# Kernel tuning notes

Measured on AMD Instinct MI355X. Metric: run time of the kernel, lower is better.

The kernel has to match this reference:

```python
import jax, jax.numpy as jnp
import numpy as np

B, L, D = 4, 2048, 512


def setup_inputs() -> dict:
    key = jax.random.key(0)
    ks = jax.random.split(key, 12)
    f32 = jnp.float32
    mk = lambda k, s: jax.random.normal(k, s, dtype=f32)
    # xavier-uniform-ish init scale for the linear weights
    w_qkv_lim = np.sqrt(6.0 / (6 * D + 6 * D)).astype(np.float32)
    w_out_lim = np.sqrt(6.0 / (2 * D + 2 * D)).astype(np.float32)
    return {
        "q_real": mk(ks[0], (B, L, D)),
        "q_imag": mk(ks[1], (B, L, D)),
        "k_real": mk(ks[2], (B, L, D)),
        "k_imag": mk(ks[3], (B, L, D)),
        "v_real": mk(ks[4], (B, L, D)),
        "v_imag": mk(ks[5], (B, L, D)),
        "pad_mask": jax.random.randint(ks[6], (B, L), 0, 2).astype(jnp.bool_),
        "W_qkv": jax.random.uniform(ks[7], (6 * D, 6 * D), f32, -w_qkv_lim, w_qkv_lim),
        "b_qkv": jnp.zeros((6 * D,), f32),
        "W_out": jax.random.uniform(ks[8], (2 * D, 2 * D), f32, -w_out_lim, w_out_lim),
        "b_out": jnp.zeros((2 * D,), f32),
    }


def reference(q_real, q_imag, k_real, k_imag, v_real, v_imag, pad_mask,
              W_qkv, b_qkv, W_out, b_out):
    b, l, d = q_real.shape
    # fused QKV projection over concatenated real/imag streams: [B, L, 6D]
    x = jnp.concatenate([q_real, q_imag, k_real, k_imag, v_real, v_imag], axis=-1)
    qkv = x @ W_qkv.T + b_qkv                      # torch Linear: x @ W^T + b
    qkv = qkv.reshape(b, l, 6, d)
    q_r, k_r = qkv[:, :, 0], qkv[:, :, 2]
    v_r, v_i = qkv[:, :, 4], qkv[:, :, 5]
    scale = jnp.asarray(d, jnp.float32) ** -0.5
    scores = jnp.einsum('bqd,bkd->bqk', q_r, k_r) * scale   # [B, L, L]
    scores = jnp.where(pad_mask[:, None, :], -jnp.inf, scores)
    attn = jax.nn.softmax(scores, axis=-1)         # dropout omitted (eval mode)
    out_real = jnp.einsum('bqk,bkd->bqd', attn, v_r)
    out_imag = jnp.einsum('bqk,bkd->bqd', attn, v_i)
    out = jnp.concatenate([out_real, out_imag], axis=-1) @ W_out.T + b_out
    return out[..., :d], out[..., d:]
```

## Files before the change

kernel.cpp:

```cpp
#include <hip/hip_runtime.h>
#include <cstdint>
#include <cstddef>

typedef unsigned short ushort;
typedef __attribute__((ext_vector_type(8))) short short8;
typedef __attribute__((ext_vector_type(16))) float f32x16;

__device__ __forceinline__ float bf2f(ushort u) {
  union { unsigned u; float f; } c; c.u = ((unsigned)u) << 16; return c.f;
}
__device__ __forceinline__ ushort f2bf(float f) {
  union { float f; unsigned u; } c; c.f = f;
  unsigned u = c.u;
  return (ushort)((u + 0x7fffu + ((u >> 16) & 1u)) >> 16);
}

#define G2L(g, l) __builtin_amdgcn_global_load_lds( \
    (const __attribute__((address_space(1))) void*)(g), \
    (__attribute__((address_space(3))) void*)(l), 16, 0, 0)

#define BARRIER() do { asm volatile("" ::: "memory"); __builtin_amdgcn_s_barrier(); asm volatile("" ::: "memory"); } while (0)
#define LGKM0()   do { asm volatile("s_waitcnt lgkmcnt(0)" ::: "memory"); __builtin_amdgcn_sched_barrier(0); } while (0)

struct MArgs {
  const ushort* A; int lda; long asz;
  const ushort* B; int ldb; long bsz;
  void* C; int ldc; long csz;
  int K;
  const float* bias;
  float* C2;
};

template<int MODE, int BN>
__launch_bounds__(512, 1)
__global__ void mfma_gemm(MArgs g) {
  constexpr int BM = 256;
  constexpr int WN = BN / 64;
  constexpr int WM = 8 / WN;
  constexpr int WMSZ = BM / WM;
  constexpr int MF = WMSZ / 32;
  constexpr int NBG = BN / 64;
  constexpr int LPS = 4 + NBG;

  __shared__ __attribute__((aligned(16))) ushort As[2][BM * 64];
  __shared__ __attribute__((aligned(16))) ushort Bs[2][BN * 64];

  const int tid = threadIdx.x;
  const int lane = tid & 63;
  const int wave = tid >> 6;
  const int z = blockIdx.z;

  int bx = blockIdx.x, by = blockIdx.y;
  {
    const int gx = gridDim.x;
    const int nwg = gx * gridDim.y;
    int wg = by * gx + bx;
    wg = (wg & 7) * (nwg >> 3) + (wg >> 3);
    bx = wg % gx; by = wg / gx;
  }
  const long m0 = (long)by * BM;
  const long n0 = (long)bx * BN;
  const ushort* Ab = g.A + (long)z * g.asz;
  const ushort* Bb = g.B + (long)z * g.bsz;

  const int srow = tid >> 3;
  const long skel = (long)((((tid & 7) - srow) & 7) * 8);
  const ushort* ga[4];
  const ushort* gb[NBG];
#pragma unroll
  for (int q = 0; q < 4; ++q) ga[q] = Ab + (m0 + q * 64 + srow) * (long)g.lda + skel;
#pragma unroll
  for (int q = 0; q < NBG; ++q) gb[q] = Bb + (n0 + q * 64 + srow) * (long)g.ldb + skel;

  const int l31 = lane & 31, hb = lane >> 5;
  const int wmi = wave / WN, wni = wave % WN;
  int aoff[MF], arot[MF];
#pragma unroll
  for (int mf = 0; mf < MF; ++mf) {
    const int r = wmi * WMSZ + mf * 32 + l31;
    aoff[mf] = r * 64;
    arot[mf] = (r + hb) & 7;
  }
  int boff[2], brot[2];
#pragma unroll
  for (int nf = 0; nf < 2; ++nf) {
    const int r = wni * 64 + nf * 32 + l31;
    boff[nf] = r * 64;
    brot[nf] = (r + hb) & 7;
  }

  f32x16 acc[MF][2];
#pragma unroll
  for (int mf = 0; mf < MF; ++mf)
#pragma unroll
    for (int nf = 0; nf < 2; ++nf)
#pragma unroll
      for (int r = 0; r < 16; ++r) acc[mf][nf][r] = 0.f;

  auto STAGE_A = [&](int buf, int t) {
    const long ko = (long)t * 64;
#pragma unroll
    for (int q = 0; q < 4; ++q) G2L(ga[q] + ko, &As[buf][q * 4096 + tid * 8]);
  };
  auto STAGE_B = [&](int buf, int t) {
    const long ko = (long)t * 64;
#pragma unroll
    for (int q = 0; q < NBG; ++q) G2L(gb[q] + ko, &Bs[buf][q * 4096 + tid * 8]);
  };

  STAGE_A(0, 0); STAGE_B(0, 0);
  STAGE_A(1, 1); STAGE_B(1, 1);
  asm volatile("s_waitcnt vmcnt(%0)" :: "n"(LPS) : "memory");
  BARRIER();

  const int nt = g.K >> 6;
  int cur = 0;
  for (int t = 0; t < nt; ++t) {
    const ushort* as = &As[cur][0];
    const ushort* bs = &Bs[cur][0];
    short8 av[4][MF], bv[4][2];

#define READ_H(h) do { \
  _Pragma("unroll") for (int mf = 0; mf < MF; ++mf) \
    av[h][mf] = *(const short8*)(as + aoff[mf] + (((2 * (h) + arot[mf]) & 7) << 3)); \
  _Pragma("unroll") for (int nf = 0; nf < 2; ++nf) \
    bv[h][nf] = *(const short8*)(bs + boff[nf] + (((2 * (h) + brot[nf]) & 7) << 3)); \
} while (0)
#define MFMA_H(h) do { \
  __builtin_amdgcn_s_setprio(1); \
  _Pragma("unroll") for (int mf = 0; mf < MF; ++mf) \
  _Pragma("unroll") for (int nf = 0; nf < 2; ++nf) \
    acc[mf][nf] = __builtin_amdgcn_mfma_f32_32x32x16_bf16(av[h][mf], bv[h][nf], acc[mf][nf], 0, 0, 0); \
  __builtin_amdgcn_s_setprio(0); \
} while (0)

    READ_H(0); READ_H(1);
    MFMA_H(0);
    BARRIER();

    READ_H(2); READ_H(3);
    MFMA_H(1);
    LGKM0();
    BARRIER();

    if (t + 2 < nt) STAGE_A(cur, t + 2);
    MFMA_H(2);
    BARRIER();

    if (t + 2 < nt) STAGE_B(cur, t + 2);
    MFMA_H(3);
    if (t + 1 < nt) {
      if (t + 2 < nt) asm volatile("s_waitcnt vmcnt(%0)" :: "n"(LPS) : "memory");
      else            asm volatile("s_waitcnt vmcnt(0)" ::: "memory");
      BARRIER();
    }
    cur ^= 1;
#undef READ_H
#undef MFMA_H
  }

  const int cc = l31;
  const int rbase = 4 * hb;
  ushort* Cu = (ushort*)g.C + (long)z * g.csz;
  float* Cf = (float*)g.C;
#pragma unroll
  for (int mf = 0; mf < MF; ++mf) {
#pragma unroll
    for (int nf = 0; nf < 2; ++nf) {
      const long col = n0 + wni * 64 + nf * 32 + cc;
      float bsv = 0.f;
      if (MODE == 0 || MODE == 3) bsv = g.bias[col];
#pragma unroll
      for (int r = 0; r < 16; ++r) {
        const long row = m0 + wmi * WMSZ + mf * 32 + (r & 3) + 8 * (r >> 2) + rbase;
        float v = acc[mf][nf][r] + bsv;
        if (MODE == 3) {
          float* dst = (col < 512) ? (Cf + row * 512 + col) : (g.C2 + row * 512 + (col - 512));
          *dst = v;
        } else {
          Cu[row * (long)g.ldc + col] = f2bf(v);
        }
      }
    }
  }
}

__global__ void cvt_x6(const float* x0, const float* x1, const float* x2,
                       const float* x3, const float* x4, const float* x5, ushort* X) {
  const long m = blockIdx.y;
  const int c4 = (blockIdx.x * 256 + threadIdx.x) * 4;
  const int p = c4 >> 9, d = c4 & 511;
  const float* xp;
  switch (p) {
    case 0: xp = x0; break; case 1: xp = x1; break; case 2: xp = x2; break;
    case 3: xp = x3; break; case 4: xp = x4; break; default: xp = x5; break;
  }
  float4 v = *(const float4*)(xp + m * 512 + d);
  ushort4 o; o.x = f2bf(v.x); o.y = f2bf(v.y); o.z = f2bf(v.z); o.w = f2bf(v.w);
  *(ushort4*)(X + m * 3072 + c4) = o;
}

__device__ __forceinline__ int chunk_map(int c) { return (c == 0) ? 0 : (c == 1) ? 2 : (c == 2) ? 4 : 5; }

__global__ void cvt_w4(const float* W, ushort* Wq4) {
  const long r = blockIdx.y;
  const int c4 = (blockIdx.x * 256 + threadIdx.x) * 4;
  const long wr = (long)chunk_map((int)(r >> 9)) * 512 + (r & 511);
  float4 v = *(const float4*)(W + wr * 3072 + c4);
  ushort4 o; o.x = f2bf(v.x); o.y = f2bf(v.y); o.z = f2bf(v.z); o.w = f2bf(v.w);
  *(ushort4*)(Wq4 + r * 3072 + c4) = o;
}

__global__ void cvt_wout(const float* W, ushort* Wo) {
  const long r = blockIdx.y;
  const int c4 = threadIdx.x * 4;
  float4 v = *(const float4*)(W + r * 1024 + c4);
  ushort4 o; o.x = f2bf(v.x); o.y = f2bf(v.y); o.z = f2bf(v.z); o.w = f2bf(v.w);
  *(ushort4*)(Wo + r * 1024 + c4) = o;
}

__global__ void mk_bias4(const float* bqkv, float* b4) {
  const int n = blockIdx.x * 256 + threadIdx.x;
  b4[n] = bqkv[chunk_map(n >> 9) * 512 + (n & 511)];
}

__global__ void transpose_v(const ushort* QKV, ushort* Vt) {
  __shared__ ushort t[64][65];
  const int tid = threadIdx.x;
  const int k0 = blockIdx.x * 64, n0 = blockIdx.y * 64, b = blockIdx.z;
  const ushort* src = QKV + (long)b * 2048 * 2048 + 1024;
#pragma unroll
  for (int i = 0; i < 16; ++i) {
    int idx = i * 256 + tid; int r = idx >> 6, c = idx & 63;
    t[r][c] = src[(long)(k0 + r) * 2048 + (n0 + c)];
  }
  __syncthreads();
  ushort* dst = Vt + (long)b * 1024 * 2048;
#pragma unroll
  for (int i = 0; i < 16; ++i) {
    int idx = i * 256 + tid; int r = idx >> 6, c = idx & 63;
    dst[(long)(n0 + r) * 2048 + (k0 + c)] = t[c][r];
  }
}

__launch_bounds__(256)
__global__ void softmax_rows(ushort* S, const int* mask) {
  const int lane = threadIdx.x & 63;
  const int wave = threadIdx.x >> 6;
  const long row = (long)blockIdx.x * 4 + wave;
  const int* m = mask + (row >> 11) * 2048 + lane * 32;
  ushort* s = S + row * 2048 + lane * 32;
  const float scale = 0.04419417382415922f;

  short8 raw[4];
#pragma unroll
  for (int i = 0; i < 4; ++i) raw[i] = *(const short8*)(s + i * 8);
  int4 mi[8];
#pragma unroll
  for (int i = 0; i < 8; ++i) mi[i] = *(const int4*)(m + i * 4);

  float v[32];
  int mk[32];
#pragma unroll
  for (int i = 0; i < 8; ++i) {
    mk[i * 4 + 0] = mi[i].x; mk[i * 4 + 1] = mi[i].y;
    mk[i * 4 + 2] = mi[i].z; mk[i * 4 + 3] = mi[i].w;
  }
#pragma unroll
  for (int i = 0; i < 32; ++i) v[i] = bf2f((ushort)raw[i >> 3][i & 7]) * scale;

  float mx = -INFINITY;
#pragma unroll
  for (int i = 0; i < 32; ++i) if (!mk[i]) mx = fmaxf(mx, v[i]);
#pragma unroll
  for (int off = 32; off; off >>= 1) mx = fmaxf(mx, __shfl_xor(mx, off));

  float sum = 0.f;
#pragma unroll
  for (int i = 0; i < 32; ++i) {
    float e = mk[i] ? 0.f : __expf(v[i] - mx);
    v[i] = e;
    sum += e;
  }
#pragma unroll
  for (int off = 32; off; off >>= 1) sum += __shfl_xor(sum, off);

  float r = 1.f / sum;
  short8 out[4];
#pragma unroll
  for (int i = 0; i < 32; ++i) out[i >> 3][i & 7] = (short)f2bf(v[i] * r);
#pragma unroll
  for (int i = 0; i < 4; ++i) *(short8*)(s + i * 8) = out[i];
}

extern "C" void kernel_launch(void* const* d_in, const int* in_sizes, int n_in,
                              void* d_out, int out_size, void* d_ws, size_t ws_size,
                              hipStream_t stream) {
  const float* qr = (const float*)d_in[0];
  const float* qi = (const float*)d_in[1];
  const float* kr = (const float*)d_in[2];
  const float* ki = (const float*)d_in[3];
  const float* vr = (const float*)d_in[4];
  const float* vi = (const float*)d_in[5];
  const int* pm = (const int*)d_in[6];
  const float* Wqkv = (const float*)d_in[7];
  const float* bqkv = (const float*)d_in[8];
  const float* Wout = (const float*)d_in[9];
  const float* bout = (const float*)d_in[10];
  float* out = (float*)d_out;

  char* base = (char*)d_ws;
  ushort* QKV   = (ushort*)(base);
  ushort* Wq4   = (ushort*)(base + 33554432);
  ushort* Wo    = (ushort*)(base + 46137344);
  float*  b4    = (float*) (base + 48234496);
  char*   uni   = base + 48242688;
  ushort* Xbf   = (ushort*)(uni);
  ushort* Vt    = (ushort*)(uni);
  ushort* S     = (ushort*)(uni + 16777216);
  ushort* AO    = (ushort*)(uni + 50331648);

  cvt_x6<<<dim3(3, 8192), 256, 0, stream>>>(qr, qi, kr, ki, vr, vi, Xbf);
  cvt_w4<<<dim3(3, 2048), 256, 0, stream>>>(Wqkv, Wq4);
  cvt_wout<<<dim3(1, 1024), 256, 0, stream>>>(Wout, Wo);
  mk_bias4<<<8, 256, 0, stream>>>(bqkv, b4);

  {
    MArgs a{};
    a.A = Xbf; a.lda = 3072; a.asz = 0;
    a.B = Wq4; a.ldb = 3072; a.bsz = 0;
    a.C = QKV; a.ldc = 2048; a.csz = 0;
    a.K = 3072; a.bias = b4;
    mfma_gemm<0, 256><<<dim3(8, 32, 1), 512, 0, stream>>>(a);
  }

  transpose_v<<<dim3(32, 16, 4), 256, 0, stream>>>(QKV, Vt);

  {
    MArgs a{};
    a.A = QKV;        a.lda = 2048; a.asz = (long)2048 * 2048;
    a.B = QKV + 512;  a.ldb = 2048; a.bsz = (long)2048 * 2048;
    a.C = S;          a.ldc = 2048; a.csz = (long)2048 * 2048;
    a.K = 512;
    mfma_gemm<1, 256><<<dim3(8, 8, 4), 512, 0, stream>>>(a);
  }

  softmax_rows<<<2048, 256, 0, stream>>>(S, pm);

  {
    MArgs a{};
    a.A = S;  a.lda = 2048; a.asz = (long)2048 * 2048;
    a.B = Vt; a.ldb = 2048; a.bsz = (long)1024 * 2048;
    a.C = AO; a.ldc = 1024; a.csz = (long)2048 * 1024;
    a.K = 2048;
    mfma_gemm<2, 128><<<dim3(8, 8, 4), 512, 0, stream>>>(a);
  }

  {
    MArgs a{};
    a.A = AO; a.lda = 1024; a.asz = 0;
    a.B = Wo; a.ldb = 1024; a.bsz = 0;
    a.C = out; a.ldc = 512; a.csz = 0;
    a.C2 = out + (long)8192 * 512;
    a.K = 1024; a.bias = bout;
    mfma_gemm<3, 128><<<dim3(8, 32, 1), 512, 0, stream>>>(a);
  }
}
```

Baseline: 404.8 us.

## Restructure GEMM main loop into per-k-slice windows for two waves per SIMD

Raises the launch bound to allow two workgroups per CU and rewrites the K loop so each 16-wide k-slice loads its fragments, issues the next tile's stage, synchronises, then runs MFMAs. Prefetch depth drops from two tiles ahead to one, and fragment registers are scoped per window to cut register pressure. The aim is to hide latency through occupancy rather than deep software pipelining. The risk is that the shared memory footprint (256x64 A plus B, double buffered) may not fit two blocks per CU, and the extra barriers and shallower prefetch can expose load latency.

Result: no change. 408.6 us (+1.0%).

```diff
diff --git a/kernel.cpp b/kernel.cpp
--- a/kernel.cpp
+++ b/kernel.cpp
@@ -32,7 +32,7 @@
 };
 
 template<int MODE, int BN>
-__launch_bounds__(512, 1)
+__launch_bounds__(512, 2)
 __global__ void mfma_gemm(MArgs g) {
   constexpr int BM = 256;
   constexpr int WN = BN / 64;
@@ -40,7 +40,6 @@
   constexpr int WMSZ = BM / WM;
   constexpr int MF = WMSZ / 32;
   constexpr int NBG = BN / 64;
-  constexpr int LPS = 4 + NBG;
 
   __shared__ __attribute__((aligned(16))) ushort As[2][BM * 64];
   __shared__ __attribute__((aligned(16))) ushort Bs[2][BN * 64];
@@ -109,54 +108,42 @@
   };
 
   STAGE_A(0, 0); STAGE_B(0, 0);
-  STAGE_A(1, 1); STAGE_B(1, 1);
-  asm volatile("s_waitcnt vmcnt(%0)" :: "n"(LPS) : "memory");
+  asm volatile("s_waitcnt vmcnt(0)" ::: "memory");
   BARRIER();
 
   const int nt = g.K >> 6;
-  int cur = 0;
   for (int t = 0; t < nt; ++t) {
-    const ushort* as = &As[cur][0];
-    const ushort* bs = &Bs[cur][0];
-    short8 av[4][MF], bv[4][2];
-
-#define READ_H(h) do { \
-  _Pragma("unroll") for (int mf = 0; mf < MF; ++mf) \
-    av[h][mf] = *(const short8*)(as + aoff[mf] + (((2 * (h) + arot[mf]) & 7) << 3)); \
-  _Pragma("unroll") for (int nf = 0; nf < 2; ++nf) \
-    bv[h][nf] = *(const short8*)(bs + boff[nf] + (((2 * (h) + brot[nf]) & 7) << 3)); \
-} while (0)
-#define MFMA_H(h) do { \
-  __builtin_amdgcn_s_setprio(1); \
-  _Pragma("unroll") for (int mf = 0; mf < MF; ++mf) \
-  _Pragma("unroll") for (int nf = 0; nf < 2; ++nf) \
-    acc[mf][nf] = __builtin_amdgcn_mfma_f32_32x32x16_bf16(av[h][mf], bv[h][nf], acc[mf][nf], 0, 0, 0); \
-  __builtin_amdgcn_s_setprio(0); \
-} while (0)
-
-    READ_H(0); READ_H(1);
-    MFMA_H(0);
-    BARRIER();
-
-    READ_H(2); READ_H(3);
-    MFMA_H(1);
-    LGKM0();
-    BARRIER();
-
-    if (t + 2 < nt) STAGE_A(cur, t + 2);
-    MFMA_H(2);
-    BARRIER();
-
-    if (t + 2 < nt) STAGE_B(cur, t + 2);
-    MFMA_H(3);
-    if (t + 1 < nt) {
-      if (t + 2 < nt) asm volatile("s_waitcnt vmcnt(%0)" :: "n"(LPS) : "memory");
-      else            asm volatile("s_waitcnt vmcnt(0)" ::: "memory");
-      BARRIER();
-    }
-    cur ^= 1;
-#undef READ_H
-#undef MFMA_H
+    const int c = t & 1;
+    const ushort* as = &As[c][0];
+    const ushort* bs = &Bs[c][0];
+
+#define WIN(h, STG, POST) do { \
+      short8 avv[MF], bvv[2]; \
+      _Pragma("unroll") for (int mf = 0; mf < MF; ++mf) \
+        avv[mf] = *(const short8*)(as + aoff[mf] + (((2 * (h) + arot[mf]) & 7) << 3)); \
+      _Pragma("unroll") for (int nf = 0; nf < 2; ++nf) \
+        bvv[nf] = *(const short8*)(bs + boff[nf] + (((2 * (h) + brot[nf]) & 7) << 3)); \
+      STG; \
+      BARRIER(); \
+      LGKM0(); \
+      __builtin_amdgcn_s_setprio(1); \
+      _Pragma("unroll") for (int mf = 0; mf < MF; ++mf) \
+      _Pragma("unroll") for (int nf = 0; nf < 2; ++nf) \
+        acc[mf][nf] = __builtin_amdgcn_mfma_f32_32x32x16_bf16(avv[mf], bvv[nf], acc[mf][nf], 0, 0, 0); \
+      __builtin_amdgcn_s_setprio(0); \
+      POST; \
+    } while (0)
+
+    WIN(0, { if (t + 1 < nt) STAGE_A(c ^ 1, t + 1); }, BARRIER());
+    WIN(1, { if (t + 1 < nt) STAGE_B(c ^ 1, t + 1); }, BARRIER());
+    WIN(2, {}, BARRIER());
+    WIN(3, {}, {
+      if (t + 1 < nt) {
+        asm volatile("s_waitcnt vmcnt(0)" ::: "memory");
+        BARRIER();
+      }
+    });
+#undef WIN
   }
 
   const int cc = l31;
```
